# Kernel optimization log

Measured on AMD Instinct MI355X. Metric: run time of the kernel, lower is better.

## Reference

```python
import jax, jax.numpy as jnp
import numpy as np

B, L, D_MODEL, N_HEADS = 2, 2048, 1024, 16
D_K = D_MODEL // N_HEADS  # 64
THETA = 10000.0


def setup_inputs() -> dict:
    key = jax.random.key(0)
    k1, k2, k3 = jax.random.split(key, 3)
    std_qkv = (2.0 / (D_MODEL + 3 * D_MODEL)) ** 0.5
    std_out = (2.0 / (D_MODEL + D_MODEL)) ** 0.5
    X = jax.random.normal(k1, (B, L, D_MODEL), dtype=jnp.float32)
    Wqkv = jax.random.truncated_normal(k2, -3.0, 3.0, (3 * D_MODEL, D_MODEL), dtype=jnp.float32) * std_qkv
    Wout = jax.random.truncated_normal(k3, -3.0, 3.0, (D_MODEL, D_MODEL), dtype=jnp.float32) * std_out
    token_positions = jnp.arange(B * L, dtype=jnp.int64 if jax.config.jax_enable_x64 else jnp.int32).reshape(B, L)
    return {"X": X, "token_positions": token_positions, "Wqkv": Wqkv, "Wout": Wout}


def _rope(X, pos):
    # X: (b, h, l, d_k); pos: (b, l)
    k = jnp.arange(D_K // 2, dtype=jnp.float32)
    inv_freq = 1.0 / (THETA ** (2.0 * k / D_K))          # (d_k/2,)
    ang = pos[..., None].astype(jnp.float32) * inv_freq  # (b, l, d_k/2)
    cos = jnp.repeat(jnp.cos(ang), 2, axis=-1)[:, None, :, :].astype(X.dtype)  # (b,1,l,d_k)
    sin = jnp.repeat(jnp.sin(ang), 2, axis=-1)[:, None, :, :].astype(X.dtype)
    # interleaved rotation: (x0,x1,x2,x3,...) -> (-x1,x0,-x3,x2,...)
    X_rot = jnp.stack([-X[..., 1::2], X[..., ::2]], axis=-1).reshape(X.shape)
    return X * cos + X_rot * sin


def reference(X, token_positions, Wqkv, Wout):
    b, l, _ = X.shape
    qkv = jnp.einsum('bld,ed->ble', X, Wqkv)  # (b, l, 3*d_model)
    Q, K, V = jnp.split(qkv, 3, axis=-1)
    to_heads = lambda t: t.reshape(b, l, N_HEADS, D_K).transpose(0, 2, 1, 3)  # (b,h,l,dk)
    Q, K, V = to_heads(Q), to_heads(K), to_heads(V)
    Q = _rope(Q, token_positions)
    K = _rope(K, token_positions)
    scores = jnp.einsum('bhqd,bhkd->bhqk', Q, K) / np.float32(np.sqrt(D_K))
    causal = jnp.tril(jnp.ones((l, l), dtype=bool))  # (l, l)
    scores = jnp.where(causal[None, None], scores.astype(jnp.float32), -jnp.inf)
    weights = jax.nn.softmax(scores, axis=-1).astype(X.dtype)
    out = jnp.einsum('bhqk,bhkd->bhqd', weights, V)
    out = out.transpose(0, 2, 1, 3).reshape(b, l, D_MODEL)
    return jnp.einsum('bld,od->blo', out, Wout)
```

## Files before the change

### kernel.cpp

```cpp
#include <hip/hip_runtime.h>
#include <stdint.h>
#include <stddef.h>
#include <math.h>

#define DEVINL __device__ __forceinline__

typedef __attribute__((ext_vector_type(8))) __bf16 bf16x8;
typedef __attribute__((ext_vector_type(4))) float f32x4;
typedef __attribute__((ext_vector_type(4))) unsigned short us4;
typedef __attribute__((ext_vector_type(8))) unsigned short us8;
typedef __attribute__((ext_vector_type(4))) short short4v;

typedef __attribute__((address_space(1))) unsigned int as1_uint;
typedef __attribute__((address_space(3))) unsigned int as3_uint;

constexpr int SEQ    = 2048;
constexpr int DMODEL = 1024;
constexpr int MTOT   = 4096;
constexpr int NQKV   = 3072;
constexpr int DKH    = 64;

constexpr size_t OFF_XBF  = 0;
constexpr size_t OFF_WQKV = OFF_XBF  + (size_t)MTOT * DMODEL * 2;
constexpr size_t OFF_WOUT = OFF_WQKV + (size_t)NQKV * DMODEL * 2;
constexpr size_t OFF_Q    = OFF_WOUT + (size_t)DMODEL * DMODEL * 2;
constexpr size_t OFF_K    = OFF_Q    + (size_t)MTOT * DMODEL * 2;
constexpr size_t OFF_VT   = OFF_K    + (size_t)MTOT * DMODEL * 2;
constexpr size_t OFF_O    = OFF_VT   + (size_t)MTOT * DMODEL * 2;
constexpr size_t OFF_ROPE = OFF_O    + (size_t)MTOT * DMODEL * 2;

constexpr float QSCALE = 0.125f * 1.4426950408889634f;

DEVINL unsigned short f2bf(float f) {
  unsigned int u = __float_as_uint(f);
  u += 0x7fffu + ((u >> 16) & 1u);
  return (unsigned short)(u >> 16);
}

DEVINL float fexp2(float x) { return __builtin_amdgcn_exp2f(x); }

DEVINL void gld_lds16(const unsigned short* g, unsigned short* s) {
  __builtin_amdgcn_global_load_lds((as1_uint*)g, (as3_uint*)s, 16, 0, 0);
}

__global__ __launch_bounds__(256) void prep_kernel(
    const float* __restrict__ X, const float* __restrict__ Wqkv,
    const float* __restrict__ Wout, const int* __restrict__ pos,
    unsigned short* __restrict__ xbf, unsigned short* __restrict__ wqkvbf,
    unsigned short* __restrict__ woutbf, float2* __restrict__ rope) {
  const int t = blockIdx.x * 256 + threadIdx.x;
  if (t < MTOT * 32) {
    const int m = t >> 5, ip = t & 31;
    const float freq = powf(10000.0f, -(float)(2 * ip) / 64.0f);
    const float ang = (float)pos[m] * freq;
    float sv, cv;
    sincosf(ang, &sv, &cv);
    rope[t] = make_float2(cv, sv);
  }
  const int NX = MTOT * DMODEL, NW1 = NQKV * DMODEL, NW2 = DMODEL * DMODEL;
  const int e = t * 4;
  const float* src;
  unsigned short* dst;
  if (e < NX) { src = X + e; dst = xbf + e; }
  else if (e < NX + NW1) { src = Wqkv + (e - NX); dst = wqkvbf + (e - NX); }
  else if (e < NX + NW1 + NW2) { src = Wout + (e - NX - NW1); dst = woutbf + (e - NX - NW1); }
  else return;
  const float4 v = *(const float4*)src;
  us4 o = { f2bf(v.x), f2bf(v.y), f2bf(v.z), f2bf(v.w) };
  *(us4*)dst = o;
}

template <int MODE>
__global__ __launch_bounds__(512) void gemm_kernel(
    const unsigned short* __restrict__ A, const unsigned short* __restrict__ Bw,
    unsigned short* __restrict__ q_out, unsigned short* __restrict__ k_out,
    unsigned short* __restrict__ vt_out, const float2* __restrict__ rope,
    float* __restrict__ f_out) {
  constexpr int K = DMODEL;
  __shared__ __align__(16) unsigned short As[2][2][128 * 32];
  __shared__ __align__(16) unsigned short Bs[2][2][128 * 32];
  const int tid = threadIdx.x;
  const int l = tid & 63, w = tid >> 6;
  const bool producer = (w >= 4);
  const int w4 = w & 3;
  const int g = l >> 4, l15 = l & 15;

  constexpr int GX  = (MODE == 0) ? 24 : 8;
  constexpr int CHN = (MODE == 0) ? 12 : 4;
  const int lid = blockIdx.x + GX * blockIdx.y;
  const int xcd = lid & 7;
  const int sc  = lid >> 3;
  const int bm = (xcd & 3) * 8 + (sc & 7);
  const int bn = (xcd >> 2) * CHN + (sc >> 3);
  const int m0 = bm * 128, n0 = bn * 128;
  const int wm = w4 >> 1, wn = w4 & 1;

  const unsigned short* ag = A  + (size_t)(m0 + w4 * 16 + (l >> 2)) * K + (l & 3) * 8;
  const unsigned short* bg = Bw + (size_t)(n0 + w4 * 16 + (l >> 2)) * K + (l & 3) * 8;

  auto STAGE = [&](int bb, int kt) {
#pragma unroll
    for (int kk = 0; kk < 2; ++kk) {
      const unsigned short* a0 = ag + kt * 64 + kk * 32;
      const unsigned short* b0 = bg + kt * 64 + kk * 32;
      unsigned short* as0 = &As[bb][kk][0] + w4 * 512;
      unsigned short* bs0 = &Bs[bb][kk][0] + w4 * 512;
      gld_lds16(a0, as0);
      gld_lds16(a0 + (size_t)64 * K, as0 + 2048);
      gld_lds16(b0, bs0);
      gld_lds16(b0 + (size_t)64 * K, bs0 + 2048);
    }
  };

  const f32x4 zf = {0.f, 0.f, 0.f, 0.f};
  f32x4 acc[4][4];
#pragma unroll
  for (int i = 0; i < 4; ++i)
#pragma unroll
    for (int j = 0; j < 4; ++j) acc[i][j] = zf;

  if (producer) STAGE(0, 0);
  __syncthreads();
  int cur = 0;

  for (int kt = 0; kt < K / 64; ++kt) {
    if (producer) {
      if (kt + 1 < K / 64) STAGE(cur ^ 1, kt + 1);
    } else {
      bf16x8 af[4][2], bf[4][2];
#pragma unroll
      for (int i = 0; i < 4; ++i)
#pragma unroll
        for (int kk = 0; kk < 2; ++kk) {
          af[i][kk] = *(const bf16x8*)(&As[cur][kk][0] + (wm * 64 + i * 16 + l15) * 32 + g * 8);
          bf[i][kk] = *(const bf16x8*)(&Bs[cur][kk][0] + (wn * 64 + i * 16 + l15) * 32 + g * 8);
        }
#pragma unroll
      for (int i = 0; i < 4; ++i)
#pragma unroll
        for (int j = 0; j < 4; ++j) {
          acc[i][j] = __builtin_amdgcn_mfma_f32_16x16x32_bf16(af[i][0], bf[j][0], acc[i][j], 0, 0, 0);
          acc[i][j] = __builtin_amdgcn_mfma_f32_16x16x32_bf16(af[i][1], bf[j][1], acc[i][j], 0, 0, 0);
        }
    }
    __syncthreads();
    cur ^= 1;
  }

  if (producer) return;

  if constexpr (MODE == 0) {
    const int region = n0 >> 10;
    if (region <= 1) {
      unsigned short* outb = (region == 0) ? q_out : k_out;
      const float qs = (region == 0) ? QSCALE : 1.0f;
#pragma unroll
      for (int i = 0; i < 4; ++i) {
        const int mb = m0 + wm * 64 + i * 16 + g * 4;
#pragma unroll
        for (int j = 0; j < 4; ++j) {
          const int n = n0 + wn * 64 + j * 16 + l15;
          const int ncol = n & 1023;
          const int ip = (n & 63) >> 1;
          const float sgn = (n & 1) ? 1.f : -1.f;
#pragma unroll
          for (int r = 0; r < 4; ++r) {
            const int m = mb + r;
            const float v = acc[i][j][r];
            const float p = __shfl_xor(v, 1);
            const float2 cs = rope[m * 32 + ip];
            const float o = (v * cs.x + sgn * p * cs.y) * qs;
            outb[(size_t)m * DMODEL + ncol] = f2bf(o);
          }
        }
      }
    } else {
#pragma unroll
      for (int i = 0; i < 4; ++i) {
        const int mb = m0 + wm * 64 + i * 16 + g * 4;
        const int b = mb >> 11;
        const int lseq = mb & 2047;
#pragma unroll
        for (int j = 0; j < 4; ++j) {
          const int n = n0 + wn * 64 + j * 16 + l15;
          const int hd = n - 2048;
          us4 o = { f2bf(acc[i][j][0]), f2bf(acc[i][j][1]), f2bf(acc[i][j][2]), f2bf(acc[i][j][3]) };
          *(us4*)(vt_out + (size_t)(b * DMODEL + hd) * SEQ + lseq) = o;
        }
      }
    }
  } else {
#pragma unroll
    for (int i = 0; i < 4; ++i) {
      const int mb = m0 + wm * 64 + i * 16 + g * 4;
#pragma unroll
      for (int j = 0; j < 4; ++j) {
        const int n = n0 + wn * 64 + j * 16 + l15;
#pragma unroll
        for (int r = 0; r < 4; ++r) f_out[(size_t)(mb + r) * DMODEL + n] = acc[i][j][r];
      }
    }
  }
}

__global__ __launch_bounds__(512) void attn_kernel(
    const unsigned short* __restrict__ Qb, const unsigned short* __restrict__ Kb,
    const unsigned short* __restrict__ Vt, unsigned short* __restrict__ Ob) {
  __shared__ __align__(16) unsigned short kv[2][2][4096];
  __shared__ __align__(16) unsigned short Olds[4][16][72];
  const int tid = threadIdx.x;
  const int l = tid & 63;
  const int wfull = tid >> 6;
  const bool producer = (wfull >= 4);
  const int w = wfull & 3;
  const int g = l >> 4, q15 = l & 15;
  const int ptid = tid & 255;

  const int lid = blockIdx.x + 16 * blockIdx.y;
  const int xcd = lid & 7;
  const int slot = lid >> 3;
  const int bh = xcd * 4 + (slot & 3);
  const int j = slot >> 2;

  const int b = bh >> 4, h = bh & 15;
  const int tA = 31 - j;
  const int tB = j;

  bf16x8 qA0{}, qA1{}, qB0{}, qB1{};
  if (!producer) {
    const unsigned short* qpA = Qb + (size_t)(b * SEQ + tA * 64 + w * 16 + q15) * DMODEL + h * DKH + g * 8;
    const unsigned short* qpB = Qb + (size_t)(b * SEQ + tB * 64 + w * 16 + q15) * DMODEL + h * DKH + g * 8;
    qA0 = *(const bf16x8*)qpA; qA1 = *(const bf16x8*)(qpA + 32);
    qB0 = *(const bf16x8*)qpB; qB1 = *(const bf16x8*)(qpB + 32);
  }
  const int qselA = tA * 64 + w * 16 + q15;
  const int qselB = tB * 64 + w * 16 + q15;

  const int rS = ptid >> 3;
  const int cS = (((ptid & 7) * 16) ^ ((rS & 7) << 4)) >> 1;
  const unsigned short* pKg = Kb + (size_t)(b * SEQ + rS) * DMODEL + h * DKH + cS;
  const unsigned short* pVg = Vt + (size_t)(b * DMODEL + h * DKH + rS) * SEQ + cS;

  const int srow = (q15 & 7) << 4;
  const int oc0 = (srow ^ (g * 16)) >> 1;
  const int oc1 = (srow ^ (g * 16 + 64)) >> 1;
  int vc[4];
#pragma unroll
  for (int blk = 0; blk < 4; ++blk) vc[blk] = ((blk * 32 + 8 * g) ^ srow) >> 1;

  const f32x4 zf = {0.f, 0.f, 0.f, 0.f};
  float mrun = -1e30f, lrun = 0.f;
  f32x4 ot[4];
#pragma unroll
  for (int d = 0; d < 4; ++d) ot[d] = zf;

  auto STAGE = [&](int bb, int k0) {
    unsigned short* lk = &kv[bb][0][0] + w * 512;
    unsigned short* lv = &kv[bb][1][0] + w * 512;
    gld_lds16(pKg + (size_t)k0 * DMODEL, lk);
    gld_lds16(pKg + (size_t)(k0 + 32) * DMODEL, lk + 2048);
    gld_lds16(pVg + k0, lv);
    gld_lds16(pVg + (size_t)32 * SEQ + k0, lv + 2048);
  };

  auto STORE = [&](int qt) {
    if (!producer) {
      float lr = lrun;
      lr += __shfl_xor(lr, 16);
      lr += __shfl_xor(lr, 32);
      const float inv = 1.0f / lr;
#pragma unroll
      for (int d = 0; d < 4; ++d) {
        us4 o = { f2bf(ot[d][0] * inv), f2bf(ot[d][1] * inv), f2bf(ot[d][2] * inv), f2bf(ot[d][3] * inv) };
        *(us4*)&Olds[w][q15][d * 16 + g * 4] = o;
      }
    }
    __syncthreads();
    if (!producer) {
      const int r = l >> 2;
      const int c = (l & 3) * 16;
      const us8 v0 = *(const us8*)&Olds[w][r][c];
      const us8 v1 = *(const us8*)&Olds[w][r][c + 8];
      unsigned short* ob = Ob + (size_t)(b * SEQ + qt * 64 + w * 16 + r) * DMODEL + h * DKH + c;
      *(us8*)ob = v0;
      *(us8*)(ob + 8) = v1;
    }
  };

  auto ITER = [&](int cur, int kb0, bf16x8 qf0, bf16x8 qf1, int qsel, bool domask) {
    const unsigned short* lkb = &kv[cur][0][0] + q15 * 64;
    const unsigned short* lvb = &kv[cur][1][0] + q15 * 64;

    float sp[4][4];
    float mt = -1e30f;
#pragma unroll
    for (int blk = 0; blk < 4; ++blk) {
      const bf16x8 kf0 = *(const bf16x8*)(lkb + blk * 1024 + oc0);
      const bf16x8 kf1 = *(const bf16x8*)(lkb + blk * 1024 + oc1);
      f32x4 c = zf;
      c = __builtin_amdgcn_mfma_f32_16x16x32_bf16(kf0, qf0, c, 0, 0, 0);
      c = __builtin_amdgcn_mfma_f32_16x16x32_bf16(kf1, qf1, c, 0, 0, 0);
#pragma unroll
      for (int r = 0; r < 4; ++r) {
        float s = c[r];
        if (domask && (kb0 + blk * 16 + g * 4 + r > qsel)) s = -1e30f;
        sp[blk][r] = s;
        mt = fmaxf(mt, s);
      }
    }
    mt = fmaxf(mt, __shfl_xor(mt, 16));
    mt = fmaxf(mt, __shfl_xor(mt, 32));

    const bool defer = __all(mt - mrun <= 8.0f);
    float mnew, alpha;
    if (defer) { mnew = mrun; alpha = 1.0f; }
    else { mnew = fmaxf(mrun, mt); alpha = fexp2(mrun - mnew); }

    float rs = 0.f;
#pragma unroll
    for (int blk = 0; blk < 4; ++blk)
#pragma unroll
      for (int r = 0; r < 4; ++r) {
        const float p = fexp2(sp[blk][r] - mnew);
        sp[blk][r] = p;
        rs += p;
      }
    if (defer) {
      lrun += rs;
    } else {
      lrun = lrun * alpha + rs;
      mrun = mnew;
#pragma unroll
      for (int d = 0; d < 4; ++d) ot[d] *= alpha;
    }

    short4v pfb[4];
#pragma unroll
    for (int blk = 0; blk < 4; ++blk) {
      union { __bf16 hh[4]; short4v v; } pk;
      pk.hh[0] = (__bf16)sp[blk][0];
      pk.hh[1] = (__bf16)sp[blk][1];
      pk.hh[2] = (__bf16)sp[blk][2];
      pk.hh[3] = (__bf16)sp[blk][3];
      pfb[blk] = pk.v;
    }

    __builtin_amdgcn_s_setprio(1);
#pragma unroll
    for (int dt = 0; dt < 4; ++dt) {
      const unsigned short* vrow = lvb + dt * 1024;
      f32x4 o = ot[dt];
#pragma unroll
      for (int blk = 0; blk < 4; ++blk) {
        const short4v vf = *(const short4v*)(vrow + vc[blk]);
        o = __builtin_amdgcn_mfma_f32_16x16x16bf16_1k(vf, pfb[blk], o, 0, 0, 0);
      }
      ot[dt] = o;
    }
    __builtin_amdgcn_s_setprio(0);
  };

  if (producer) STAGE(0, 0);
  __syncthreads();
  int cur = 0;

  for (int i = 0; i < tA; ++i) {
    if (producer) STAGE(cur ^ 1, (i + 1) * 64);
    else ITER(cur, i * 64, qA0, qA1, qselA, false);
    __syncthreads();
    cur ^= 1;
  }
  if (producer) STAGE(cur ^ 1, 0);
  else ITER(cur, tA * 64, qA0, qA1, qselA, true);
  STORE(tA);
  if (!producer) {
    mrun = -1e30f; lrun = 0.f;
#pragma unroll
    for (int d = 0; d < 4; ++d) ot[d] = zf;
  }
  __syncthreads();
  cur ^= 1;

  for (int i = 0; i < tB; ++i) {
    if (producer) STAGE(cur ^ 1, (i + 1) * 64);
    else ITER(cur, i * 64, qB0, qB1, qselB, false);
    __syncthreads();
    cur ^= 1;
  }
  if (!producer) ITER(cur, tB * 64, qB0, qB1, qselB, true);
  STORE(tB);
}

extern "C" void kernel_launch(void* const* d_in, const int* in_sizes, int n_in,
                              void* d_out, int out_size, void* d_ws, size_t ws_size,
                              hipStream_t stream) {
  const float* X = (const float*)d_in[0];
  const int* pos = (const int*)d_in[1];
  const float* Wqkv = (const float*)d_in[2];
  const float* Wout = (const float*)d_in[3];
  char* ws = (char*)d_ws;
  unsigned short* xbf    = (unsigned short*)(ws + OFF_XBF);
  unsigned short* wqkvbf = (unsigned short*)(ws + OFF_WQKV);
  unsigned short* woutbf = (unsigned short*)(ws + OFF_WOUT);
  unsigned short* qb     = (unsigned short*)(ws + OFF_Q);
  unsigned short* kbuf   = (unsigned short*)(ws + OFF_K);
  unsigned short* vt     = (unsigned short*)(ws + OFF_VT);
  unsigned short* ob     = (unsigned short*)(ws + OFF_O);
  float2* rope           = (float2*)(ws + OFF_ROPE);

  prep_kernel<<<8192, 256, 0, stream>>>(X, Wqkv, Wout, pos, xbf, wqkvbf, woutbf, rope);
  gemm_kernel<0><<<dim3(NQKV / 128, MTOT / 128), 512, 0, stream>>>(
      xbf, wqkvbf, qb, kbuf, vt, rope, nullptr);
  attn_kernel<<<dim3(16, 32), 512, 0, stream>>>(qb, kbuf, vt, ob);
  gemm_kernel<1><<<dim3(DMODEL / 128, MTOT / 128), 512, 0, stream>>>(
      ob, woutbf, nullptr, nullptr, nullptr, nullptr, (float*)d_out);
}
```

Measured before the change: 105.9 us.

## Triple-buffer K/V LDS staging in attention with partial vmcnt waits

The attention kernel's K/V shared-memory ring goes from two to three stages, so producer waves prefetch two tiles ahead across both query-tile phases using a unified step counter. Full __syncthreads are replaced with raw s_barrier plus targeted waits: producers wait only for the older load group (vmcnt(4)), consumers wait on lgkmcnt. The aim is to hide global-to-LDS latency behind MFMA compute and cut barrier stalls. It raises LDS use per block, which could lower occupancy, and the hand-written waitcnt logic is fragile.

```diff
diff --git a/kernel.cpp b/kernel.cpp
--- a/kernel.cpp
+++ b/kernel.cpp
@@ -206,7 +206,7 @@
 __global__ __launch_bounds__(512) void attn_kernel(
     const unsigned short* __restrict__ Qb, const unsigned short* __restrict__ Kb,
     const unsigned short* __restrict__ Vt, unsigned short* __restrict__ Ob) {
-  __shared__ __align__(16) unsigned short kv[2][2][4096];
+  __shared__ __align__(16) unsigned short kv[3][2][4096];
   __shared__ __align__(16) unsigned short Olds[4][16][72];
   const int tid = threadIdx.x;
   const int l = tid & 63;
@@ -254,6 +254,8 @@
 #pragma unroll
   for (int d = 0; d < 4; ++d) ot[d] = zf;
 
+  auto KN = [&](int s) { return (s <= tA) ? s : (s - tA - 1); };
+
   auto STAGE = [&](int bb, int k0) {
     unsigned short* lk = &kv[bb][0][0] + w * 512;
     unsigned short* lv = &kv[bb][1][0] + w * 512;
@@ -263,6 +265,18 @@
     gld_lds16(pVg + (size_t)32 * SEQ + k0, lv + 2048);
   };
 
+  auto BAR = [&](int s) {
+    if (producer) {
+      if (s + 2 < 33) asm volatile("s_waitcnt vmcnt(4)" ::: "memory");
+      else            asm volatile("s_waitcnt vmcnt(0)" ::: "memory");
+    } else {
+      asm volatile("s_waitcnt lgkmcnt(0)" ::: "memory");
+    }
+    __builtin_amdgcn_sched_barrier(0);
+    __builtin_amdgcn_s_barrier();
+    __builtin_amdgcn_sched_barrier(0);
+  };
+
   auto STORE = [&](int qt) {
     if (!producer) {
       float lr = lrun;
@@ -275,7 +289,10 @@
         *(us4*)&Olds[w][q15][d * 16 + g * 4] = o;
       }
     }
-    __syncthreads();
+    asm volatile("s_waitcnt lgkmcnt(0)" ::: "memory");
+    __builtin_amdgcn_sched_barrier(0);
+    __builtin_amdgcn_s_barrier();
+    __builtin_amdgcn_sched_barrier(0);
     if (!producer) {
       const int r = l >> 2;
       const int c = (l & 3) * 16;
@@ -360,34 +377,38 @@
     __builtin_amdgcn_s_setprio(0);
   };
 
-  if (producer) STAGE(0, 0);
-  __syncthreads();
-  int cur = 0;
-
-  for (int i = 0; i < tA; ++i) {
-    if (producer) STAGE(cur ^ 1, (i + 1) * 64);
-    else ITER(cur, i * 64, qA0, qA1, qselA, false);
-    __syncthreads();
-    cur ^= 1;
-  }
-  if (producer) STAGE(cur ^ 1, 0);
-  else ITER(cur, tA * 64, qA0, qA1, qselA, true);
+  if (producer) {
+    STAGE(0, 0);
+    STAGE(1, KN(1) * 64);
+    asm volatile("s_waitcnt vmcnt(4)" ::: "memory");
+  }
+  __builtin_amdgcn_sched_barrier(0);
+  __builtin_amdgcn_s_barrier();
+  __builtin_amdgcn_sched_barrier(0);
+
+  int s = 0;
+  for (int i = 0; i < tA; ++i, ++s) {
+    if (producer) { if (s + 2 < 33) STAGE((s + 2) % 3, KN(s + 2) * 64); }
+    else ITER(s % 3, i * 64, qA0, qA1, qselA, false);
+    BAR(s);
+  }
+  if (producer) { if (s + 2 < 33) STAGE((s + 2) % 3, KN(s + 2) * 64); }
+  else ITER(s % 3, tA * 64, qA0, qA1, qselA, true);
   STORE(tA);
   if (!producer) {
     mrun = -1e30f; lrun = 0.f;
 #pragma unroll
     for (int d = 0; d < 4; ++d) ot[d] = zf;
   }
-  __syncthreads();
-  cur ^= 1;
-
-  for (int i = 0; i < tB; ++i) {
-    if (producer) STAGE(cur ^ 1, (i + 1) * 64);
-    else ITER(cur, i * 64, qB0, qB1, qselB, false);
-    __syncthreads();
-    cur ^= 1;
-  }
-  if (!producer) ITER(cur, tB * 64, qB0, qB1, qselB, true);
+  BAR(s);
+  ++s;
+
+  for (int i = 0; i < tB; ++i, ++s) {
+    if (producer) { if (s + 2 < 33) STAGE((s + 2) % 3, KN(s + 2) * 64); }
+    else ITER(s % 3, i * 64, qB0, qB1, qselB, false);
+    BAR(s);
+  }
+  if (!producer) ITER(s % 3, tB * 64, qB0, qB1, qselB, true);
   STORE(tB);
 }
 
```

New measurement: 107.3 us. About the same (+1.4%).
